# Kernel optimization log

Measured on AMD Instinct MI355X. Metric: run time of the kernel, lower is better.

## Reference

```python
import jax, jax.numpy as jnp
import numpy as np


def _f_map(x):
    # alpha = ||x||; x normalized; append a constant-1 feature
    alpha = jnp.linalg.norm(x, axis=-1, keepdims=True)
    xn = x / jnp.maximum(alpha, 1e-12)
    ones = jnp.ones(x.shape[:-1] + (1,), x.dtype)
    return jnp.concatenate([(1.0 - 0.5 ** alpha) * xn, ones], axis=-1)


def _mh_lka(q, k, v):
    # kernelized linear attention: cumsum of k (x) v outer products along seq
    q = _f_map(q)  # (B, N, D+1)
    k = _f_map(k)
    kv = jnp.cumsum(jnp.einsum('bnd,bne->bnde', k, v), axis=1)  # (B,N,D+1,D)
    k_ = jnp.cumsum(k, axis=1)
    qk = jnp.einsum('bnd,bnd->bn', q, k_)[..., None]
    qkv = jnp.einsum('bnd,bnde->bne', q, kv)
    return qkv / qk


def _lstm(x, Wih, Whh, bih, bhh):
    # single-layer batch-first LSTM, torch gate order (i, f, g, o)
    B, H = x.shape[0], Whh.shape[1]
    bias = bih + bhh
    def step(carry, xt):
        h, c = carry
        g = xt @ Wih.T + h @ Whh.T + bias  # (B, 4H)
        i, f, gg, o = jnp.split(g, 4, axis=-1)
        c = jax.nn.sigmoid(f) * c + jax.nn.sigmoid(i) * jnp.tanh(gg)
        h = jax.nn.sigmoid(o) * jnp.tanh(c)
        return (h, c), h
    h0 = jnp.zeros((B, H), x.dtype)
    c0 = jnp.zeros((B, H), x.dtype)
    _, hs = jax.lax.scan(step, (h0, c0), x.transpose(1, 0, 2))
    return hs.transpose(1, 0, 2)


def setup_inputs() -> dict:
    in_sz, hid, n_h, out_sz = 512, 64, 8, 512
    B, N = 2, 2048
    key = jax.random.key(0)
    ks = jax.random.split(key, 10)
    s = 0.02
    f32 = jnp.float32
    return {
        'x': jax.random.normal(ks[0], (B, N, in_sz), f32),
        'Wq': jax.random.normal(ks[1], (in_sz, hid * n_h), f32) * s,
        'bq': jnp.zeros((hid * n_h,), f32),
        'Wk': jax.random.normal(ks[2], (in_sz, hid * n_h), f32) * s,
        'bk': jnp.zeros((hid * n_h,), f32),
        'Wv': jax.random.normal(ks[3], (in_sz, hid * n_h), f32) * s,
        'bv': jnp.zeros((hid * n_h,), f32),
        'Wih': jax.random.normal(ks[4], (4 * hid, hid), f32) * s,
        'Whh': jax.random.normal(ks[5], (4 * hid, hid), f32) * s,
        'bih': jnp.zeros((4 * hid,), f32),
        'bhh': jnp.zeros((4 * hid,), f32),
        'W1': jax.random.normal(ks[6], (hid * n_h, out_sz), f32) * s,
        'b1': jnp.zeros((out_sz,), f32),
        'W2': jax.random.normal(ks[7], (out_sz, out_sz), f32) * s,
        'b2': jnp.zeros((out_sz,), f32),
        'gamma': jnp.ones((out_sz,), f32),
        'beta': jnp.zeros((out_sz,), f32),
    }


def reference(x, Wq, bq, Wk, bk, Wv, bv, Wih, Whh, bih, bhh, W1, b1, W2, b2, gamma, beta):
    B, N, _ = x.shape
    H = Whh.shape[1]
    n_h = Wq.shape[1] // H
    def proj(W, b_):
        y = x @ W + b_                              # (B, N, n_h*H)
        return y.reshape(B, N, n_h, H).transpose(0, 2, 1, 3).reshape(B * n_h, N, H)
    q, k, v = proj(Wq, bq), proj(Wk, bk), proj(Wv, bv)
    o = _mh_lka(q, k, v)                            # (B*n_h, N, H)
    o = o + _lstm(o, Wih, Whh, bih, bhh)
    o = o.reshape(B, n_h, N, H).transpose(0, 2, 1, 3).reshape(B, N, n_h * H)
    o = jax.nn.gelu(o @ W1 + b1, approximate=False) @ W2 + b2
    mu = o.mean(-1, keepdims=True)
    var = o.var(-1, keepdims=True)
    return (o - mu) / jnp.sqrt(var + 1e-5) * gamma + beta
```

## Files before the change

kernel.cpp:

```cpp
#include <hip/hip_runtime.h>
#include <hip/hip_bf16.h>
#include <hip/hip_fp16.h>

using bf16 = __hip_bfloat16;
using ushort_t = unsigned short;
using uint32 = unsigned int;
typedef _Float16 f16x2 __attribute__((ext_vector_type(2)));
typedef short short8 __attribute__((ext_vector_type(8)));
typedef float floatx4 __attribute__((ext_vector_type(4)));

__device__ __forceinline__ float u2f(ushort_t u) {
  return __uint_as_float(((unsigned int)u) << 16);
}
__device__ __forceinline__ bool probe_f32(const void* graw) {
  return ((const ushort_t*)graw)[0] != 0x3F80;
}
__device__ __forceinline__ float scrub(float v) {
  return fminf(fmaxf(v, -1e4f), 1e4f);
}
__device__ __forceinline__ short f2b(float x) {
  uint32 u = __float_as_uint(x);
  return (short)((u + 0x7FFFu + ((u >> 16) & 1u)) >> 16);
}
__device__ __forceinline__ float frcp(float x) {
#if __has_builtin(__builtin_amdgcn_rcpf)
  return __builtin_amdgcn_rcpf(x);
#else
  return 1.f / x;
#endif
}
template<int CTRL>
__device__ __forceinline__ float qperm(float x) {
  return __int_as_float(__builtin_amdgcn_mov_dpp(__float_as_int(x), CTRL, 0xF, 0xF, false));
}
__device__ __forceinline__ float fdot2(uint32 a, uint32 b, float c) {
#if __has_builtin(__builtin_amdgcn_fdot2)
  return __builtin_amdgcn_fdot2(__builtin_bit_cast(f16x2, a),
                                __builtin_bit_cast(f16x2, b), c, false);
#else
  const f16x2 av = __builtin_bit_cast(f16x2, a);
  const f16x2 bv = __builtin_bit_cast(f16x2, b);
  return c + (float)av[0] * (float)bv[0] + (float)av[1] * (float)bv[1];
#endif
}

struct Ptrs { const void* p[16]; };

__global__ __launch_bounds__(256) void cvt_k(Ptrs ps, float* __restrict__ dst) {
  const int sizes[16] = {262144,512,262144,512,262144,512,16384,16384,
                         256,256,262144,512,262144,512,512,512};
  int idx = blockIdx.x * 256 + threadIdx.x;
  if (idx >= 1347840) return;
  const bool f32in = probe_f32(ps.p[14]);
  if (idx >= 1347584) {
    const int i = idx - 1347584;
    float a, b;
    if (f32in) { a = ((const float*)ps.p[8])[i]; b = ((const float*)ps.p[9])[i]; }
    else { a = u2f(((const ushort_t*)ps.p[8])[i]); b = u2f(((const ushort_t*)ps.p[9])[i]); }
    dst[idx] = a + b;
    return;
  }
  int seg = 0, off = idx;
  while (off >= sizes[seg]) { off -= sizes[seg]; seg++; }
  float v;
  if (f32in) v = ((const float*)ps.p[seg])[off];
  else       v = u2f(((const ushort_t*)ps.p[seg])[off]);
  dst[idx] = v;
}

template<int AMODE, int ACT, int BMODE, int OUT>
__global__ __launch_bounds__(256) void gemm_mfma(
    const void* __restrict__ A, const float* __restrict__ B,
    const float* __restrict__ bias, const void* __restrict__ graw,
    void* __restrict__ Cv, int M, int N, int K)
{
  __shared__ __align__(16) short As2[64][36];
  __shared__ __align__(16) short Bs2[64][36];
  const int t = threadIdx.x;
  const int row0 = blockIdx.y * 64, col0 = blockIdx.x * 64;
  const int w = t >> 6, lane = t & 63;
  const int quad = lane >> 4, lr = lane & 15;
  bool f32in = true;
  if (AMODE == 1) f32in = probe_f32(graw);

  const int am = t >> 2, akq = t & 3;
  const int bn = t & 63, bkq = t >> 6;

  floatx4 acc[4] = {{0,0,0,0},{0,0,0,0},{0,0,0,0},{0,0,0,0}};

  for (int k0 = 0; k0 < K; k0 += 32) {
    {
      const size_t aoff = (size_t)(row0 + am) * K + (k0 + akq * 8);
      short8 ap;
      if (AMODE == 0 || f32in) {
        const float4 v0 = *reinterpret_cast<const float4*>((const float*)A + aoff);
        const float4 v1 = *reinterpret_cast<const float4*>((const float*)A + aoff + 4);
        ap[0]=f2b(v0.x); ap[1]=f2b(v0.y); ap[2]=f2b(v0.z); ap[3]=f2b(v0.w);
        ap[4]=f2b(v1.x); ap[5]=f2b(v1.y); ap[6]=f2b(v1.z); ap[7]=f2b(v1.w);
      } else {
        const ushort4 u0 = *reinterpret_cast<const ushort4*>((const ushort_t*)A + aoff);
        const ushort4 u1 = *reinterpret_cast<const ushort4*>((const ushort_t*)A + aoff + 4);
        ap[0]=(short)u0.x; ap[1]=(short)u0.y; ap[2]=(short)u0.z; ap[3]=(short)u0.w;
        ap[4]=(short)u1.x; ap[5]=(short)u1.y; ap[6]=(short)u1.z; ap[7]=(short)u1.w;
      }
      *reinterpret_cast<short8*>(&As2[am][akq * 8]) = ap;
    }
    {
      short8 bpk;
      if (BMODE == 0) {
        const float* bp = B + (size_t)(k0 + bkq * 8) * N + col0 + bn;
        #pragma unroll
        for (int j = 0; j < 8; j++) bpk[j] = f2b(bp[(size_t)j * N]);
      } else {
        const float* bp = B + (size_t)(col0 + bn) * K + k0 + bkq * 8;
        const float4 v0 = *reinterpret_cast<const float4*>(bp);
        const float4 v1 = *reinterpret_cast<const float4*>(bp + 4);
        bpk[0]=f2b(v0.x); bpk[1]=f2b(v0.y); bpk[2]=f2b(v0.z); bpk[3]=f2b(v0.w);
        bpk[4]=f2b(v1.x); bpk[5]=f2b(v1.y); bpk[6]=f2b(v1.z); bpk[7]=f2b(v1.w);
      }
      *reinterpret_cast<short8*>(&Bs2[bn][bkq * 8]) = bpk;
    }
    __syncthreads();
    {
      const short8 af = *reinterpret_cast<const short8*>(&As2[w * 16 + lr][quad * 8]);
      #pragma unroll
      for (int ct = 0; ct < 4; ct++) {
        const short8 bf = *reinterpret_cast<const short8*>(&Bs2[ct * 16 + lr][quad * 8]);
        acc[ct] = __builtin_amdgcn_mfma_f32_16x16x32_bf16(af, bf, acc[ct], 0, 0, 0);
      }
    }
    __syncthreads();
  }
  #pragma unroll
  for (int ct = 0; ct < 4; ct++) {
    const int col = col0 + ct * 16 + lr;
    const float bb = bias[col];
    #pragma unroll
    for (int r = 0; r < 4; r++) {
      const int row = row0 + w * 16 + quad * 4 + r;
      float v = acc[ct][r] + bb;
      if (ACT == 1) v = 0.5f * v * (1.0f + erff(v * 0.70710678118654752f));
      if (OUT == 0) ((float*)Cv)[(size_t)row * N + col] = scrub(v);
      else ((__half*)Cv)[(size_t)row * N + col] = __float2half(scrub(v));
    }
  }
}

__global__ __launch_bounds__(256) void attn_pass1(
    const float* __restrict__ kb, const float* __restrict__ vb,
    float* __restrict__ S, float* __restrict__ kcS)
{
  const int c = blockIdx.x, bh = blockIdx.y;
  const int b = bh >> 3, hd = bh & 7;
  const int t = threadIdx.x;
  const int e = t & 63, p = t >> 6;

  __shared__ __align__(16) float kf_s[64][64];
  __shared__ __align__(16) float v_s[64][64];

  for (int r = 0; r < 16; r++) {
    const int nl = p * 16 + r;
    const size_t base = ((size_t)(b * 2048 + c * 64 + nl)) * 512 + hd * 64 + e;
    const float kr = kb[base];
    const float vr = vb[base];
    float s = kr * kr;
    #pragma unroll
    for (int off = 32; off > 0; off >>= 1) s += __shfl_xor(s, off);
    const float ak = sqrtf(s);
    kf_s[nl][e] = (1.0f - exp2f(-ak)) * frcp(fmaxf(ak, 1e-12f)) * kr;
    v_s[nl][e] = vr;
  }
  __syncthreads();

  float Sl[16], kcl[16], S64 = 0.f;
  #pragma unroll
  for (int i = 0; i < 16; i++) { Sl[i] = 0.f; kcl[i] = 0.f; }
  for (int nn = 0; nn < 64; nn++) {
    const float ve = v_s[nn][e];
    #pragma unroll
    for (int i = 0; i < 16; i++) {
      const float kfd = kf_s[nn][p * 16 + i];
      Sl[i]  += kfd * ve;
      kcl[i] += kfd;
    }
    if (p == 0) S64 += ve;
  }
  const size_t sbase = ((size_t)(bh * 32 + c)) * 4160;
  #pragma unroll
  for (int i = 0; i < 16; i++) S[sbase + (p * 16 + i) * 64 + e] = Sl[i];
  if (p == 0) S[sbase + 4096 + e] = S64;
  if (e == 0) {
    const size_t kbase = ((size_t)(bh * 32 + c)) * 64;
    #pragma unroll
    for (int i = 0; i < 16; i++) kcS[kbase + p * 16 + i] = kcl[i];
  }
}

__global__ __launch_bounds__(256) void attn_pass2(
    float* __restrict__ S, float* __restrict__ kcS)
{
  const int bh = blockIdx.y;
  const int idx = blockIdx.x * 256 + threadIdx.x;
  if (idx < 4160) {
    const size_t base = (size_t)bh * 32 * 4160 + idx;
    float v[32];
    #pragma unroll
    for (int cc = 0; cc < 32; cc++) v[cc] = S[base + (size_t)cc * 4160];
    float run = 0.f;
    #pragma unroll
    for (int cc = 0; cc < 32; cc++) { const float tmp = v[cc]; v[cc] = run; run += tmp; }
    #pragma unroll
    for (int cc = 0; cc < 32; cc++) S[base + (size_t)cc * 4160] = v[cc];
  }
  if (blockIdx.x == 0 && threadIdx.x < 64) {
    const size_t base = (size_t)bh * 32 * 64 + threadIdx.x;
    float v[32];
    #pragma unroll
    for (int cc = 0; cc < 32; cc++) v[cc] = kcS[base + (size_t)cc * 64];
    float run = 0.f;
    #pragma unroll
    for (int cc = 0; cc < 32; cc++) { const float tmp = v[cc]; v[cc] = run; run += tmp; }
    #pragma unroll
    for (int cc = 0; cc < 32; cc++) kcS[base + (size_t)cc * 64] = v[cc];
  }
}

__global__ __launch_bounds__(256) void attn_pass3(
    const float* __restrict__ qb, const float* __restrict__ kb, const float* __restrict__ vb,
    const float* __restrict__ S, const float* __restrict__ kcS,
    float* __restrict__ ao)
{
  const int c = blockIdx.x, bh = blockIdx.y;
  const int b = bh >> 3, hd = bh & 7;
  const int t = threadIdx.x;
  const int e = t & 63, p = t >> 6;

  __shared__ __align__(16) float qf_s[64][64], kf_s[64][64], v_s[64][64];
  __shared__ __align__(16) float accp_s[2][4][64];
  __shared__ float qkp_s[2][4];

  for (int r = 0; r < 16; r++) {
    const int nl = p * 16 + r;
    const size_t base = ((size_t)(b * 2048 + c * 64 + nl)) * 512 + hd * 64 + e;
    const float qr = qb[base];
    const float kr = kb[base];
    const float vr = vb[base];
    float sq = qr * qr, sk = kr * kr;
    #pragma unroll
    for (int off = 32; off > 0; off >>= 1) {
      sq += __shfl_xor(sq, off);
      sk += __shfl_xor(sk, off);
    }
    const float aq = sqrtf(sq), ak = sqrtf(sk);
    qf_s[nl][e] = (1.0f - exp2f(-aq)) * frcp(fmaxf(aq, 1e-12f)) * qr;
    kf_s[nl][e] = (1.0f - exp2f(-ak)) * frcp(fmaxf(ak, 1e-12f)) * kr;
    v_s[nl][e] = vr;
  }

  float Sl[16], kcl[16], S64;
  {
    const size_t sbase = ((size_t)(bh * 32 + c)) * 4160;
    #pragma unroll
    for (int i = 0; i < 16; i++) Sl[i] = S[sbase + (p * 16 + i) * 64 + e];
    S64 = S[sbase + 4096 + e];
    const size_t kbase = ((size_t)(bh * 32 + c)) * 64;
    #pragma unroll
    for (int i = 0; i < 16; i++) kcl[i] = kcS[kbase + p * 16 + i];
  }
  __syncthreads();

  for (int nn = 0; nn < 64; nn++) {
    const int n = c * 64 + nn;
    const int buf = nn & 1;
    const float ve = v_s[nn][e];
    float accp = 0.f, qkp = 0.f;
    #pragma unroll
    for (int i = 0; i < 16; i++) {
      const float kfd = kf_s[nn][p * 16 + i];
      const float qfd = qf_s[nn][p * 16 + i];
      Sl[i]  += kfd * ve;
      accp   += qfd * Sl[i];
      kcl[i] += kfd;
      qkp    += qfd * kcl[i];
    }
    if (p == 0) {
      S64  += ve;
      accp += S64;
      qkp  += (float)(n + 1);
    }
    accp_s[buf][p][e] = accp;
    if (e == 0) qkp_s[buf][p] = qkp;
    __syncthreads();
    if (t < 64) {
      const float num = accp_s[buf][0][t] + accp_s[buf][1][t] +
                        accp_s[buf][2][t] + accp_s[buf][3][t];
      float den = qkp_s[buf][0] + qkp_s[buf][1] + qkp_s[buf][2] + qkp_s[buf][3];
      den = fmaxf(den, 1e-6f);
      ao[((size_t)(bh * 2048 + n)) * 64 + t] = scrub(num / den);
    }
  }
}

__global__ __attribute__((amdgpu_flat_work_group_size(256, 256), amdgpu_waves_per_eu(1, 1)))
void lstm_k(
    const float* __restrict__ ao, const __half* __restrict__ G,
    const float* __restrict__ Whhf, float* __restrict__ y1)
{
  const int bh = blockIdx.x;
  const int b = bh >> 3, hd = bh & 7;
  const int t = threadIdx.x;
  const int gate = t & 3;
  const int e = t >> 2;
  const int jg = gate * 64 + e;
  const bool isG = (gate == 2);
  const bool owner = (gate == 0);

  __shared__ __align__(16) _Float16 hh[2][64];
  __shared__ __align__(16) float ao_s[2][16 * 64];

  uint32 w[32];
  {
    const float4* wp = reinterpret_cast<const float4*>(Whhf + (size_t)jg * 64);
    #pragma unroll
    for (int i = 0; i < 16; i++) {
      const float4 v = wp[i];
      f16x2 p0; p0[0] = (_Float16)v.x; p0[1] = (_Float16)v.y;
      f16x2 p1; p1[0] = (_Float16)v.z; p1[1] = (_Float16)v.w;
      w[i * 2 + 0] = __builtin_bit_cast(uint32, p0);
      w[i * 2 + 1] = __builtin_bit_cast(uint32, p1);
    }
  }
  #pragma unroll
  for (int i = 0; i < 32; i++) asm volatile("" : "+v"(w[i]));

  float c = 0.f;
  if (t < 64) hh[0][t] = (_Float16)0.f;

  const size_t aobase = (size_t)bh * 2048 * 64;
  const size_t gbase  = (size_t)bh * 2048 * 256;
  const ushort_t* Gu = reinterpret_cast<const ushort_t*>(G);

  float gcur[16];
  {
    const float4 a0 = *reinterpret_cast<const float4*>(ao + aobase + t * 4);
    *reinterpret_cast<float4*>(&ao_s[0][t * 4]) = a0;
    #pragma unroll
    for (int j = 0; j < 16; j++) {
      const ushort_t gu = Gu[gbase + (size_t)j * 256 + jg];
      gcur[j] = (float)__builtin_bit_cast(_Float16, gu);
    }
  }
  __syncthreads();

  for (int ch = 0; ch < 128; ch++) {
    const int buf = ch & 1;
    float4 a1; ushort_t gn2[16];
    if (ch + 1 < 128) {
      a1 = *reinterpret_cast<const float4*>(ao + aobase + (size_t)(ch + 1) * 1024 + t * 4);
      #pragma unroll
      for (int j = 0; j < 16; j++)
        gn2[j] = Gu[gbase + (size_t)(ch + 1) * 4096 + (size_t)j * 256 + jg];
    }
    #pragma unroll
    for (int nn = 0; nn < 16; nn++) {
      const int n = ch * 16 + nn;
      const int hb = n & 1;
      const float gin = gcur[nn];
      const uint4* hp = reinterpret_cast<const uint4*>(&hh[hb][0]);
      float d0 = 0.f, d1 = 0.f, d2 = 0.f, d3 = 0.f;
      #pragma unroll
      for (int q = 0; q < 8; q++) {
        const uint4 h4 = hp[q];
        d0 = fdot2(w[q * 4 + 0], h4.x, d0);
        d1 = fdot2(w[q * 4 + 1], h4.y, d1);
        d2 = fdot2(w[q * 4 + 2], h4.z, d2);
        d3 = fdot2(w[q * 4 + 3], h4.w, d3);
      }
      const float g = gin + (d0 + d1) + (d2 + d3);
      const float xx = isG ? (2.f * g) : g;
      const float sg = frcp(1.0f + __expf(-xx));
      const float act = isG ? (2.f * sg - 1.f) : sg;
      const float af  = qperm<0xB1>(act);
      const float ag  = qperm<0x4E>(act);
      const float ao4 = qperm<0x1B>(act);
      if (owner) {
        c = af * c + act * ag;
        const float ex = __expf(2.f * c);
        const float tc = 1.f - 2.f * frcp(ex + 1.f);
        const float h = ao4 * tc;
        hh[1 - hb][e] = (_Float16)h;
        y1[((size_t)(b * 2048 + n)) * 512 + hd * 64 + e] =
            scrub(ao_s[buf][nn * 64 + e] + h);
      }
      if (nn == 15 && ch + 1 < 128) {
        const int nb = 1 - buf;
        *reinterpret_cast<float4*>(&ao_s[nb][t * 4]) = a1;
        #pragma unroll
        for (int j = 0; j < 16; j++)
          gcur[j] = (float)__builtin_bit_cast(_Float16, gn2[j]);
      }
      asm volatile("s_waitcnt lgkmcnt(0)\n\ts_barrier" ::: "memory");
    }
  }
}

__global__ __launch_bounds__(256) void ln_k(
    const float* __restrict__ X, const float* __restrict__ gamf,
    const float* __restrict__ betf, const void* __restrict__ graw,
    void* __restrict__ out)
{
  const int r = blockIdx.x;
  const int t = threadIdx.x;
  const bool f32out = probe_f32(graw);
  const float a = X[(size_t)r * 512 + t];
  const float b = X[(size_t)r * 512 + 256 + t];
  float s1 = a + b, s2 = a * a + b * b;
  #pragma unroll
  for (int off = 32; off > 0; off >>= 1) {
    s1 += __shfl_xor(s1, off);
    s2 += __shfl_xor(s2, off);
  }
  __shared__ float sh1[4], sh2[4];
  if ((t & 63) == 0) { sh1[t >> 6] = s1; sh2[t >> 6] = s2; }
  __syncthreads();
  const float tot1 = sh1[0] + sh1[1] + sh1[2] + sh1[3];
  const float tot2 = sh2[0] + sh2[1] + sh2[2] + sh2[3];
  const float mu = tot1 * (1.0f / 512.0f);
  const float var = fmaxf(tot2 * (1.0f / 512.0f) - mu * mu, 0.f);
  const float rs = rsqrtf(var + 1e-5f);
  const float o0 = scrub((a - mu) * rs * gamf[t]       + betf[t]);
  const float o1 = scrub((b - mu) * rs * gamf[256 + t] + betf[256 + t]);
  if (f32out) {
    ((float*)out)[(size_t)r * 512 + t]       = o0;
    ((float*)out)[(size_t)r * 512 + 256 + t] = o1;
  } else {
    ((bf16*)out)[(size_t)r * 512 + t]       = __float2bfloat16(o0);
    ((bf16*)out)[(size_t)r * 512 + 256 + t] = __float2bfloat16(o1);
  }
}

extern "C" void kernel_launch(void* const* d_in, const int* in_sizes, int n_in,
                              void* d_out, int out_size, void* d_ws, size_t ws_size,
                              hipStream_t stream) {
  const void* x    = d_in[0];
  const void* graw = d_in[15];

  float* ws  = (float*)d_ws;
  float* q   = ws;
  float* kb  = q   + 2097152;
  float* v   = kb  + 2097152;
  float* ao  = v   + 2097152;
  float* S   = ao  + 2097152;
  float* kcS = S   + 2129920;
  float* cvt = kcS + 32768;
  float* Wqf  = cvt;            float* bqf  = cvt + 262144;
  float* Wkf  = cvt + 262656;   float* bkf  = cvt + 524800;
  float* Wvf  = cvt + 525312;   float* bvf  = cvt + 787456;
  float* Wihf = cvt + 787968;   float* Whhf = cvt + 804352;
  float* W1f  = cvt + 821248;   float* b1f  = cvt + 1083392;
  float* W2f  = cvt + 1083904;  float* b2f_ = cvt + 1346048;
  float* gamf = cvt + 1346560;  float* betf = cvt + 1347072;
  float* bsum = cvt + 1347584;
  __half* G = (__half*)kb;
  float* y1 = q;
  float* f1 = kb;
  float* f2 = v;

  Ptrs ps;
  for (int i = 0; i < 16; i++) ps.p[i] = d_in[i + 1];

  cvt_k<<<(1347840 + 255) / 256, 256, 0, stream>>>(ps, cvt);

  const dim3 gg(8, 64);
  gemm_mfma<1, 0, 0, 0><<<gg, 256, 0, stream>>>(x, Wqf, bqf, graw, q,  4096, 512, 512);
  gemm_mfma<1, 0, 0, 0><<<gg, 256, 0, stream>>>(x, Wkf, bkf, graw, kb, 4096, 512, 512);
  gemm_mfma<1, 0, 0, 0><<<gg, 256, 0, stream>>>(x, Wvf, bvf, graw, v,  4096, 512, 512);
  attn_pass1<<<dim3(32, 16), 256, 0, stream>>>(kb, v, S, kcS);
  attn_pass2<<<dim3(17, 16), 256, 0, stream>>>(S, kcS);
  attn_pass3<<<dim3(32, 16), 256, 0, stream>>>(q, kb, v, S, kcS, ao);
  gemm_mfma<0, 0, 1, 1><<<dim3(4, 512), 256, 0, stream>>>(ao, Wihf, bsum, graw, G, 32768, 256, 64);
  lstm_k<<<16, 256, 0, stream>>>(ao, G, Whhf, y1);
  gemm_mfma<0, 1, 0, 0><<<gg, 256, 0, stream>>>(y1, W1f, b1f, graw, f1, 4096, 512, 512);
  gemm_mfma<0, 0, 0, 0><<<gg, 256, 0, stream>>>(f1, W2f, b2f_, graw, f2, 4096, 512, 512);
  ln_k<<<4096, 256, 0, stream>>>(f2, gamf, betf, graw, d_out);
}
```

Before: 923.4 us.

## Restructure LSTM kernel into one compute wave and one prefetch wave

The recurrent kernel used to give each of 256 threads one gate row, exchange activations with DPP, and hit a block-wide barrier on every timestep. Now a single wave holds all four gate rows of Whh per hidden unit in registers (128 VGPRs) and runs the 16 steps of a chunk without any barrier. A second wave stages the next chunk's input-gate values and attention outputs into double-buffered LDS, and the two waves synchronise only once per chunk. The trade is four times the dot-product work per thread on the serial path, in exchange for removing the per-step cross-wave barrier and the DPP shuffles.

```diff
diff --git a/kernel.cpp b/kernel.cpp
--- a/kernel.cpp
+++ b/kernel.cpp
@@ -28,10 +28,6 @@
 #else
   return 1.f / x;
 #endif
-}
-template<int CTRL>
-__device__ __forceinline__ float qperm(float x) {
-  return __int_as_float(__builtin_amdgcn_mov_dpp(__float_as_int(x), CTRL, 0xF, 0xF, false));
 }
 __device__ __forceinline__ float fdot2(uint32 a, uint32 b, float c) {
 #if __has_builtin(__builtin_amdgcn_fdot2)
@@ -301,7 +297,7 @@
   }
 }
 
-__global__ __attribute__((amdgpu_flat_work_group_size(256, 256), amdgpu_waves_per_eu(1, 1)))
+__global__ __attribute__((amdgpu_flat_work_group_size(128, 128), amdgpu_waves_per_eu(1, 1)))
 void lstm_k(
     const float* __restrict__ ao, const __half* __restrict__ G,
     const float* __restrict__ Whhf, float* __restrict__ y1)
@@ -309,98 +305,111 @@
   const int bh = blockIdx.x;
   const int b = bh >> 3, hd = bh & 7;
   const int t = threadIdx.x;
-  const int gate = t & 3;
-  const int e = t >> 2;
-  const int jg = gate * 64 + e;
-  const bool isG = (gate == 2);
-  const bool owner = (gate == 0);
-
-  __shared__ __align__(16) _Float16 hh[2][64];
-  __shared__ __align__(16) float ao_s[2][16 * 64];
-
-  uint32 w[32];
-  {
-    const float4* wp = reinterpret_cast<const float4*>(Whhf + (size_t)jg * 64);
-    #pragma unroll
-    for (int i = 0; i < 16; i++) {
-      const float4 v = wp[i];
-      f16x2 p0; p0[0] = (_Float16)v.x; p0[1] = (_Float16)v.y;
-      f16x2 p1; p1[0] = (_Float16)v.z; p1[1] = (_Float16)v.w;
-      w[i * 2 + 0] = __builtin_bit_cast(uint32, p0);
-      w[i * 2 + 1] = __builtin_bit_cast(uint32, p1);
-    }
-  }
-  #pragma unroll
-  for (int i = 0; i < 32; i++) asm volatile("" : "+v"(w[i]));
-
-  float c = 0.f;
-  if (t < 64) hh[0][t] = (_Float16)0.f;
+  const int e = t & 63;
+  const int wid = t >> 6;
+
+  __shared__ __align__(16) _Float16 hh[64];
+  __shared__ __align__(16) float ao_s[2][1024];
+  __shared__ __align__(16) __half G_s[2][4096];
 
   const size_t aobase = (size_t)bh * 2048 * 64;
   const size_t gbase  = (size_t)bh * 2048 * 256;
   const ushort_t* Gu = reinterpret_cast<const ushort_t*>(G);
 
-  float gcur[16];
-  {
-    const float4 a0 = *reinterpret_cast<const float4*>(ao + aobase + t * 4);
-    *reinterpret_cast<float4*>(&ao_s[0][t * 4]) = a0;
-    #pragma unroll
-    for (int j = 0; j < 16; j++) {
-      const ushort_t gu = Gu[gbase + (size_t)j * 256 + jg];
-      gcur[j] = (float)__builtin_bit_cast(_Float16, gu);
-    }
+  uint32 w0[32], w1[32], w2[32], w3[32];
+  float c = 0.f;
+  if (wid == 0) {
+    #pragma unroll
+    for (int g = 0; g < 4; g++) {
+      uint32* wg = (g == 0) ? w0 : (g == 1) ? w1 : (g == 2) ? w2 : w3;
+      const float4* wp = reinterpret_cast<const float4*>(Whhf + (size_t)(g * 64 + e) * 64);
+      #pragma unroll
+      for (int i = 0; i < 16; i++) {
+        const float4 v = wp[i];
+        f16x2 p0; p0[0] = (_Float16)v.x; p0[1] = (_Float16)v.y;
+        f16x2 p1; p1[0] = (_Float16)v.z; p1[1] = (_Float16)v.w;
+        wg[i * 2 + 0] = __builtin_bit_cast(uint32, p0);
+        wg[i * 2 + 1] = __builtin_bit_cast(uint32, p1);
+      }
+    }
+    #pragma unroll
+    for (int i = 0; i < 32; i++) {
+      asm volatile("" : "+v"(w0[i])); asm volatile("" : "+v"(w1[i]));
+      asm volatile("" : "+v"(w2[i])); asm volatile("" : "+v"(w3[i]));
+    }
+    hh[e] = (_Float16)0.f;
+  } else {
+    const uint4* gs = reinterpret_cast<const uint4*>(Gu + gbase);
+    uint4* gd = reinterpret_cast<uint4*>(&G_s[0][0]);
+    #pragma unroll
+    for (int j = 0; j < 8; j++) gd[j * 64 + e] = gs[j * 64 + e];
+    const float4* as_ = reinterpret_cast<const float4*>(ao + aobase);
+    float4* ad = reinterpret_cast<float4*>(&ao_s[0][0]);
+    #pragma unroll
+    for (int j = 0; j < 4; j++) ad[j * 64 + e] = as_[j * 64 + e];
   }
   __syncthreads();
 
   for (int ch = 0; ch < 128; ch++) {
     const int buf = ch & 1;
-    float4 a1; ushort_t gn2[16];
-    if (ch + 1 < 128) {
-      a1 = *reinterpret_cast<const float4*>(ao + aobase + (size_t)(ch + 1) * 1024 + t * 4);
+    if (wid == 0) {
       #pragma unroll
-      for (int j = 0; j < 16; j++)
-        gn2[j] = Gu[gbase + (size_t)(ch + 1) * 4096 + (size_t)j * 256 + jg];
-    }
-    #pragma unroll
-    for (int nn = 0; nn < 16; nn++) {
-      const int n = ch * 16 + nn;
-      const int hb = n & 1;
-      const float gin = gcur[nn];
-      const uint4* hp = reinterpret_cast<const uint4*>(&hh[hb][0]);
-      float d0 = 0.f, d1 = 0.f, d2 = 0.f, d3 = 0.f;
-      #pragma unroll
-      for (int q = 0; q < 8; q++) {
-        const uint4 h4 = hp[q];
-        d0 = fdot2(w[q * 4 + 0], h4.x, d0);
-        d1 = fdot2(w[q * 4 + 1], h4.y, d1);
-        d2 = fdot2(w[q * 4 + 2], h4.z, d2);
-        d3 = fdot2(w[q * 4 + 3], h4.w, d3);
-      }
-      const float g = gin + (d0 + d1) + (d2 + d3);
-      const float xx = isG ? (2.f * g) : g;
-      const float sg = frcp(1.0f + __expf(-xx));
-      const float act = isG ? (2.f * sg - 1.f) : sg;
-      const float af  = qperm<0xB1>(act);
-      const float ag  = qperm<0x4E>(act);
-      const float ao4 = qperm<0x1B>(act);
-      if (owner) {
-        c = af * c + act * ag;
-        const float ex = __expf(2.f * c);
-        const float tc = 1.f - 2.f * frcp(ex + 1.f);
-        const float h = ao4 * tc;
-        hh[1 - hb][e] = (_Float16)h;
-        y1[((size_t)(b * 2048 + n)) * 512 + hd * 64 + e] =
-            scrub(ao_s[buf][nn * 64 + e] + h);
-      }
-      if (nn == 15 && ch + 1 < 128) {
+      for (int nn = 0; nn < 16; nn++) {
+        const int n = ch * 16 + nn;
+        const float gi0 = (float)G_s[buf][nn * 256 + e];
+        const float gi1 = (float)G_s[buf][nn * 256 + 64 + e];
+        const float gi2 = (float)G_s[buf][nn * 256 + 128 + e];
+        const float gi3 = (float)G_s[buf][nn * 256 + 192 + e];
+        const float a_cur = ao_s[buf][nn * 64 + e];
+        const uint4* hv = reinterpret_cast<const uint4*>(&hh[0]);
+        float d0a = 0.f, d0b = 0.f, d1a = 0.f, d1b = 0.f;
+        float d2a = 0.f, d2b = 0.f, d3a = 0.f, d3b = 0.f;
+        #pragma unroll
+        for (int q = 0; q < 8; q++) {
+          const uint4 h4 = hv[q];
+          d0a = fdot2(w0[q*4+0], h4.x, d0a); d0b = fdot2(w0[q*4+1], h4.y, d0b);
+          d0a = fdot2(w0[q*4+2], h4.z, d0a); d0b = fdot2(w0[q*4+3], h4.w, d0b);
+          d1a = fdot2(w1[q*4+0], h4.x, d1a); d1b = fdot2(w1[q*4+1], h4.y, d1b);
+          d1a = fdot2(w1[q*4+2], h4.z, d1a); d1b = fdot2(w1[q*4+3], h4.w, d1b);
+          d2a = fdot2(w2[q*4+0], h4.x, d2a); d2b = fdot2(w2[q*4+1], h4.y, d2b);
+          d2a = fdot2(w2[q*4+2], h4.z, d2a); d2b = fdot2(w2[q*4+3], h4.w, d2b);
+          d3a = fdot2(w3[q*4+0], h4.x, d3a); d3b = fdot2(w3[q*4+1], h4.y, d3b);
+          d3a = fdot2(w3[q*4+2], h4.z, d3a); d3b = fdot2(w3[q*4+3], h4.w, d3b);
+        }
+        const float xi = gi0 + d0a + d0b;
+        const float xf = gi1 + d1a + d1b;
+        const float xg = gi2 + d2a + d2b;
+        const float xo = gi3 + d3a + d3b;
+        const float si = frcp(1.f + __expf(-xi));
+        const float sf = frcp(1.f + __expf(-xf));
+        const float tg = 2.f * frcp(1.f + __expf(-2.f * xg)) - 1.f;
+        const float so = frcp(1.f + __expf(-xo));
+        c = sf * c + si * tg;
+        const float tc = 1.f - 2.f * frcp(__expf(2.f * c) + 1.f);
+        const float h = so * tc;
+        hh[e] = (_Float16)h;
+        y1[((size_t)(b * 2048 + n)) * 512 + hd * 64 + e] = scrub(a_cur + h);
+      }
+    } else {
+      if (ch + 1 < 128) {
         const int nb = 1 - buf;
-        *reinterpret_cast<float4*>(&ao_s[nb][t * 4]) = a1;
-        #pragma unroll
-        for (int j = 0; j < 16; j++)
-          gcur[j] = (float)__builtin_bit_cast(_Float16, gn2[j]);
-      }
-      asm volatile("s_waitcnt lgkmcnt(0)\n\ts_barrier" ::: "memory");
-    }
+        uint4 gv[8]; float4 av[4];
+        const uint4* gs = reinterpret_cast<const uint4*>(Gu + gbase + (size_t)(ch + 1) * 4096);
+        #pragma unroll
+        for (int j = 0; j < 8; j++) gv[j] = gs[j * 64 + e];
+        const float4* as_ = reinterpret_cast<const float4*>(ao + aobase + (size_t)(ch + 1) * 1024);
+        #pragma unroll
+        for (int j = 0; j < 4; j++) av[j] = as_[j * 64 + e];
+        uint4* gd = reinterpret_cast<uint4*>(&G_s[nb][0]);
+        #pragma unroll
+        for (int j = 0; j < 8; j++) gd[j * 64 + e] = gv[j];
+        float4* ad = reinterpret_cast<float4*>(&ao_s[nb][0]);
+        #pragma unroll
+        for (int j = 0; j < 4; j++) ad[j * 64 + e] = av[j];
+      }
+      asm volatile("s_waitcnt lgkmcnt(0)" ::: "memory");
+    }
+    asm volatile("s_barrier" ::: "memory");
   }
 }
 
@@ -479,7 +488,7 @@
   attn_pass2<<<dim3(17, 16), 256, 0, stream>>>(S, kcS);
   attn_pass3<<<dim3(32, 16), 256, 0, stream>>>(q, kb, v, S, kcS, ao);
   gemm_mfma<0, 0, 1, 1><<<dim3(4, 512), 256, 0, stream>>>(ao, Wihf, bsum, graw, G, 32768, 256, 64);
-  lstm_k<<<16, 256, 0, stream>>>(ao, G, Whhf, y1);
+  lstm_k<<<16, 128, 0, stream>>>(ao, G, Whhf, y1);
   gemm_mfma<0, 1, 0, 0><<<gg, 256, 0, stream>>>(y1, W1f, b1f, graw, f1, 4096, 512, 512);
   gemm_mfma<0, 0, 0, 0><<<gg, 256, 0, stream>>>(f1, W2f, b2f_, graw, f2, 4096, 512, 512);
   ln_k<<<4096, 256, 0, stream>>>(f2, gamf, betf, graw, d_out);
```

Result: slower. 1.095 ms (+18.6%).
